# Performance work log

Measured on AMD Instinct MI355X. Metric: run time of the kernel, lower is better.

## Reference

```python
import jax, jax.numpy as jnp
import numpy as np

N = 100000        # nodes
E = 1600000       # edges (before self-loops)
IN_CH = 256       # input features
HEADS = 8         # conv1 heads; per-head dim also 8 (GATConv(in, heads, heads=heads))
HID = 8
NCLASS = 64
SLOPE = 0.2       # PyG leaky_relu negative slope


def _gat_conv(x, edge_index, W, att_src, att_dst, bias, heads, ch, concat):
    """PyG GATConv (eval mode): gather -> leaky_relu score -> segment softmax -> scatter."""
    n = x.shape[0]
    src, dst = edge_index[0], edge_index[1]
    h = (x @ W).reshape(n, heads, ch)                      # [N, H, C]
    a_src = jnp.einsum('nhc,hc->nh', h, att_src)           # [N, H]
    a_dst = jnp.einsum('nhc,hc->nh', h, att_dst)
    alpha = jax.nn.leaky_relu(a_src[src] + a_dst[dst], SLOPE)  # [E, H]
    # segment softmax over destination node
    amax = jax.ops.segment_max(alpha, dst, num_segments=n)     # [N, H]
    ex = jnp.exp(alpha - amax[dst])
    denom = jax.ops.segment_sum(ex, dst, num_segments=n)
    coef = ex / (denom[dst] + 1e-16)                           # [E, H]
    out = jax.ops.segment_sum(coef[:, :, None] * h[src], dst, num_segments=n)  # [N, H, C]
    if concat:
        out = out.reshape(n, heads * ch)
    else:
        out = out.mean(axis=1)
    return out + bias


def _add_self_loops(edge_index, n):
    loop = jnp.arange(n, dtype=edge_index.dtype)
    return jnp.concatenate([edge_index, jnp.stack([loop, loop])], axis=1)


def setup_inputs() -> dict:
    key = jax.random.key(0)
    ks = jax.random.split(key, 10)
    g = lambda k, shp, s: (jax.random.normal(k, shp, jnp.float32) * s)
    return {
        'x': jax.random.normal(ks[0], (N, IN_CH), jnp.float32),
        'edge_index': jax.random.randint(ks[1], (2, E), 0, N, dtype=jnp.int64),
        'W1': g(ks[2], (IN_CH, HEADS * HID), 1.0 / np.sqrt(IN_CH)),
        'att_src1': g(ks[3], (HEADS, HID), 0.3),
        'att_dst1': g(ks[4], (HEADS, HID), 0.3),
        'b1': jnp.zeros((HEADS * HID,), jnp.float32),
        'W2': g(ks[5], (HEADS * HID, NCLASS), 1.0 / np.sqrt(HEADS * HID)),
        'att_src2': g(ks[6], (1, NCLASS), 0.3),
        'att_dst2': g(ks[7], (1, NCLASS), 0.3),
        'b2': jnp.zeros((NCLASS,), jnp.float32),
    }


def reference(x, edge_index, W1, att_src1, att_dst1, b1, W2, att_src2, att_dst2, b2):
    ei = _add_self_loops(edge_index, x.shape[0])
    h = jax.nn.elu(_gat_conv(x, ei, W1, att_src1, att_dst1, b1, HEADS, HID, True))
    # dropout is a no-op in eval mode
    h = _gat_conv(h, ei, W2, att_src2, att_dst2, b2, 1, NCLASS, False)
    return jax.nn.log_softmax(h, axis=-1)
```

## Files before the change

### kernel.cpp

```cpp
#include <hip/hip_runtime.h>
#include <hip/hip_bf16.h>

#define LRELU_SLOPE 0.2f
#define NBUK 256
#define BCAP 9728
#define CH2 6144

typedef unsigned int uint;
typedef unsigned short ushort;
typedef short bt8 __attribute__((ext_vector_type(8)));
typedef float fx4 __attribute__((ext_vector_type(4)));

__device__ __forceinline__ ushort f2bf(float f) {
    uint u = __float_as_uint(f);
    return (ushort)((u + 0x7FFF + ((u >> 16) & 1)) >> 16);
}
__device__ __forceinline__ float bf2f(ushort h) {
    return __uint_as_float(((uint)h) << 16);
}

#define ACC8(e, hv) \
    acc[0] += (e) * bf2f((ushort)((hv).x & 0xffff)); \
    acc[1] += (e) * bf2f((ushort)((hv).x >> 16));    \
    acc[2] += (e) * bf2f((ushort)((hv).y & 0xffff)); \
    acc[3] += (e) * bf2f((ushort)((hv).y >> 16));    \
    acc[4] += (e) * bf2f((ushort)((hv).z & 0xffff)); \
    acc[5] += (e) * bf2f((ushort)((hv).z >> 16));    \
    acc[6] += (e) * bf2f((ushort)((hv).w & 0xffff)); \
    acc[7] += (e) * bf2f((ushort)((hv).w >> 16));

__global__ __launch_bounds__(256) void prep_init(
    const float* __restrict__ W1, const float* __restrict__ W2,
    ushort* __restrict__ WT1, ushort* __restrict__ WT2, int* __restrict__ pcur)
{
    int t = threadIdx.x;
    int idx = blockIdx.x * 256 + t;
    if (blockIdx.x == 0) pcur[t] = t * BCAP;
    if (idx < 64 * 256) {
        int c = idx >> 8, k = idx & 255;
        WT1[idx] = f2bf(W1[k * 64 + c]);
    }
    int i2 = idx - 64 * 256;
    if (i2 >= 0 && i2 < 64 * 64) {
        int c = i2 >> 6, k = i2 & 63;
        WT2[i2] = f2bf(W2[k * 64 + c]);
    }
}

__device__ __forceinline__ void partition_body(
    int bid, const int* __restrict__ ei, int E_, int ET,
    int* __restrict__ pcur, uint* __restrict__ pairs,
    int* lcnt, int* lsc, int* lplace, int* gpos)
{
    const int t = threadIdx.x;
    const int base = bid * CH2;
    const int total = min(CH2, ET - base);
    if (total <= 0) return;

    if (t < NBUK) lcnt[t] = 0;
    __syncthreads();

    uint pp[6]; int pk[6];
    #pragma unroll
    for (int i = 0; i < 6; ++i) {
        int idx = t + i * 1024;
        pk[i] = -1;
        if (idx < total) {
            int e = base + idx;
            int s, d;
            if (e < E_) { s = ei[e]; d = ei[E_ + e]; } else { s = d = e - E_; }
            pk[i] = d >> 9;
            pp[i] = (uint)s | ((uint)(d & 511) << 17);
            atomicAdd(&lcnt[pk[i]], 1);
        }
    }
    __syncthreads();

    if (t < NBUK) lsc[t] = lcnt[t];
    __syncthreads();
    for (int off = 1; off < NBUK; off <<= 1) {
        int add = 0;
        if (t < NBUK && t >= off) add = lsc[t - off];
        __syncthreads();
        if (t < NBUK) lsc[t] += add;
        __syncthreads();
    }
    if (t < NBUK) {
        int excl = lsc[t] - lcnt[t];
        lplace[t] = excl;
        int c = lcnt[t];
        gpos[t] = c ? (atomicAdd(&pcur[t], c) - excl) : 0;
    }
    __syncthreads();

    #pragma unroll
    for (int i = 0; i < 6; ++i) {
        if (pk[i] >= 0) {
            int slot = atomicAdd(&lplace[pk[i]], 1);
            pairs[gpos[pk[i]] + slot] = pp[i];
        }
    }
}

__device__ __forceinline__ void gemm1_body4(
    int gbid, const float* __restrict__ X, const ushort* __restrict__ WT,
    ushort* __restrict__ OUT, float* __restrict__ a_src, float* __restrict__ a_dst,
    const float* __restrict__ att_s, const float* __restrict__ att_d, int nrows,
    ushort* wt_l, ushort* a_l)
{
    constexpr int K = 256, LDW = K + 8, NIT = K / 32;
    const int t = threadIdx.x;
    const int tt = t & 255;
    const int base = (gbid * 4 + (t >> 8)) * 64;

    for (int idx = t * 8; idx < 64 * K; idx += 1024 * 8) {
        int r = idx / K, c = idx % K;
        *(uint4*)&wt_l[r * LDW + c] = *(const uint4*)&WT[idx];
    }

    const int w = tt >> 6, l = tt & 63;
    const int frow = l & 15;
    const int kof = (l >> 4) * 8;
    fx4 acc[4] = {};
    float4 rv0, rv1;

    auto load_tile = [&](int k0) {
        int kq = (tt & 7) * 4;
        int r0 = (tt >> 3);
        int g0 = base + r0, g1 = base + r0 + 32;
        rv0 = make_float4(0.f, 0.f, 0.f, 0.f);
        rv1 = make_float4(0.f, 0.f, 0.f, 0.f);
        if (g0 < nrows) rv0 = *(const float4*)(X + (size_t)g0 * K + k0 + kq);
        if (g1 < nrows) rv1 = *(const float4*)(X + (size_t)g1 * K + k0 + kq);
    };
    auto store_tile = [&]() {
        int kq = (tt & 7) * 4;
        int r0 = (tt >> 3);
        ushort4 o0, o1;
        o0.x = f2bf(rv0.x); o0.y = f2bf(rv0.y); o0.z = f2bf(rv0.z); o0.w = f2bf(rv0.w);
        o1.x = f2bf(rv1.x); o1.y = f2bf(rv1.y); o1.z = f2bf(rv1.z); o1.w = f2bf(rv1.w);
        *(ushort4*)&a_l[r0 * 40 + kq] = o0;
        *(ushort4*)&a_l[(r0 + 32) * 40 + kq] = o1;
    };

    load_tile(0);
    store_tile();
    for (int it = 0; it < NIT; ++it) {
        if (it + 1 < NIT) load_tile((it + 1) * 32);
        __syncthreads();
        bt8 af = *(const bt8*)&a_l[(16 * w + frow) * 40 + kof];
        #pragma unroll
        for (int g = 0; g < 4; ++g) {
            bt8 bf = *(const bt8*)&wt_l[(16 * g + frow) * LDW + it * 32 + kof];
            acc[g] = __builtin_amdgcn_mfma_f32_16x16x32_bf16(af, bf, acc[g], 0, 0, 0);
        }
        __syncthreads();
        if (it + 1 < NIT) store_tile();
    }

    const int orow0 = base + 16 * w + (l >> 4) * 4;
    const int ocol = l & 15;
    #pragma unroll
    for (int g = 0; g < 4; ++g) {
        #pragma unroll
        for (int r4 = 0; r4 < 4; ++r4) {
            int gr = orow0 + r4;
            if (gr < nrows) OUT[(size_t)gr * 64 + 16 * g + ocol] = f2bf(acc[g][r4]);
        }
    }

    float as_c[4], ad_c[4];
    #pragma unroll
    for (int g = 0; g < 4; ++g) {
        as_c[g] = att_s[16 * g + ocol];
        ad_c[g] = att_d[16 * g + ocol];
    }
    #pragma unroll
    for (int r4 = 0; r4 < 4; ++r4) {
        int gr = orow0 + r4;
        #pragma unroll
        for (int g = 0; g < 4; ++g) {
            float ps = acc[g][r4] * as_c[g];
            float pd = acc[g][r4] * ad_c[g];
            ps += __shfl_xor(ps, 1, 64); pd += __shfl_xor(pd, 1, 64);
            ps += __shfl_xor(ps, 2, 64); pd += __shfl_xor(pd, 2, 64);
            ps += __shfl_xor(ps, 4, 64); pd += __shfl_xor(pd, 4, 64);
            if ((l & 7) == 0 && gr < nrows) {
                int head = 2 * g + ((l >> 3) & 1);
                a_src[(size_t)gr * 8 + head] = ps;
                a_dst[(size_t)gr * 8 + head] = pd;
            }
        }
    }
}

__global__ __launch_bounds__(1024) void part_gemm1(
    const int* __restrict__ ei, int E_, int ET, int part_grid,
    int* __restrict__ pcur, uint* __restrict__ pairs,
    const float* __restrict__ x, const ushort* __restrict__ WT1,
    ushort* __restrict__ HB, float* __restrict__ a_s1, float* __restrict__ a_d1,
    const float* __restrict__ att_s, const float* __restrict__ att_d, int n)
{
    __shared__ int lcnt[NBUK], lsc[NBUK], lplace[NBUK], gpos[NBUK];
    __shared__ ushort wt_l[64 * 264];
    __shared__ ushort a_l4[4][64 * 40];
    if ((int)blockIdx.x < part_grid)
        partition_body(blockIdx.x, ei, E_, ET, pcur, pairs, lcnt, lsc, lplace, gpos);
    else
        gemm1_body4(blockIdx.x - part_grid, x, WT1, HB, a_s1, a_d1,
                    att_s, att_d, n, wt_l, a_l4[threadIdx.x >> 8]);
}

__global__ __launch_bounds__(1024) void phase2_build(
    const uint* __restrict__ pairs, const int* __restrict__ pcur,
    int* __restrict__ rp, int* __restrict__ ssrc, int n, int nbuk_used)
{
    __shared__ int hist[512], cur[512], psc[NBUK];
    const int k = blockIdx.x;
    const int t = threadIdx.x;
    const int beg = k * BCAP;
    const int cnt = pcur[k] - beg;
    const int dbase = k << 9;

    if (t < 512) hist[t] = 0;
    if (t < NBUK) psc[t] = (t < nbuk_used) ? (pcur[t] - t * BCAP) : 0;
    __syncthreads();
    for (int off = 1; off < NBUK; off <<= 1) {
        int add = (t < NBUK && t >= off) ? psc[t - off] : 0;
        __syncthreads();
        if (t < NBUK) psc[t] += add;
        __syncthreads();
    }
    const int bbase = k ? psc[k - 1] : 0;

    for (int i = t; i < cnt; i += 1024)
        atomicAdd(&hist[pairs[beg + i] >> 17], 1);
    __syncthreads();

    int c0 = (t < 512) ? hist[t] : 0;
    for (int off = 1; off < 512; off <<= 1) {
        int add = (t < 512 && t >= off) ? hist[t - off] : 0;
        __syncthreads();
        if (t < 512) hist[t] += add;
        __syncthreads();
    }
    if (t < 512) {
        int node = dbase + t;
        if (node < n) rp[node] = bbase + hist[t];
        cur[t] = hist[t] - c0;
    }
    __syncthreads();

    for (int i = t; i < cnt; i += 1024) {
        uint p = pairs[beg + i];
        int j = p >> 17;
        int pos = bbase + atomicAdd(&cur[j], 1);
        ssrc[pos] = (int)(p & 0x1FFFF);
    }
}

__global__ __launch_bounds__(256) void gemm2_att(
    const ushort* __restrict__ X, const ushort* __restrict__ WT,
    ushort* __restrict__ OUT, float* __restrict__ a_src, float* __restrict__ a_dst,
    const float* __restrict__ att_s, const float* __restrict__ att_d, int nrows)
{
    constexpr int K = 64, LDW = K + 8, NIT = K / 32;
    __shared__ ushort wt_l[64 * LDW];
    __shared__ ushort a_l[64 * 40];
    const int t = threadIdx.x;
    const int base = blockIdx.x * 64;

    for (int idx = t * 8; idx < 64 * K; idx += 256 * 8) {
        int r = idx / K, c = idx % K;
        *(uint4*)&wt_l[r * LDW + c] = *(const uint4*)&WT[idx];
    }

    const int w = t >> 6, l = t & 63;
    const int frow = l & 15;
    const int kof = (l >> 4) * 8;
    fx4 acc[4] = {};
    uint4 rb;

    auto load_tile = [&](int k0) {
        int r = t >> 2, kq = (t & 3) * 8;
        int gr = base + r;
        rb = make_uint4(0, 0, 0, 0);
        if (gr < nrows) rb = *(const uint4*)(X + (size_t)gr * K + k0 + kq);
    };
    auto store_tile = [&]() {
        int r = t >> 2, kq = (t & 3) * 8;
        *(uint4*)&a_l[r * 40 + kq] = rb;
    };

    load_tile(0);
    store_tile();
    for (int it = 0; it < NIT; ++it) {
        if (it + 1 < NIT) load_tile((it + 1) * 32);
        __syncthreads();
        bt8 af = *(const bt8*)&a_l[(16 * w + frow) * 40 + kof];
        #pragma unroll
        for (int g = 0; g < 4; ++g) {
            bt8 bf = *(const bt8*)&wt_l[(16 * g + frow) * LDW + it * 32 + kof];
            acc[g] = __builtin_amdgcn_mfma_f32_16x16x32_bf16(af, bf, acc[g], 0, 0, 0);
        }
        __syncthreads();
        if (it + 1 < NIT) store_tile();
    }

    const int orow0 = base + 16 * w + (l >> 4) * 4;
    const int ocol = l & 15;
    #pragma unroll
    for (int g = 0; g < 4; ++g) {
        #pragma unroll
        for (int r4 = 0; r4 < 4; ++r4) {
            int gr = orow0 + r4;
            if (gr < nrows) OUT[(size_t)gr * 64 + 16 * g + ocol] = f2bf(acc[g][r4]);
        }
    }

    float as_c[4], ad_c[4];
    #pragma unroll
    for (int g = 0; g < 4; ++g) {
        as_c[g] = att_s[16 * g + ocol];
        ad_c[g] = att_d[16 * g + ocol];
    }
    #pragma unroll
    for (int r4 = 0; r4 < 4; ++r4) {
        int gr = orow0 + r4;
        float ps = 0.f, pd = 0.f;
        #pragma unroll
        for (int g = 0; g < 4; ++g) {
            ps += acc[g][r4] * as_c[g];
            pd += acc[g][r4] * ad_c[g];
        }
        ps += __shfl_xor(ps, 1, 64); pd += __shfl_xor(pd, 1, 64);
        ps += __shfl_xor(ps, 2, 64); pd += __shfl_xor(pd, 2, 64);
        ps += __shfl_xor(ps, 4, 64); pd += __shfl_xor(pd, 4, 64);
        ps += __shfl_xor(ps, 8, 64); pd += __shfl_xor(pd, 8, 64);
        if ((l & 15) == 0 && gr < nrows) {
            a_src[gr] = ps;
            a_dst[gr] = pd;
        }
    }
}

__global__ __launch_bounds__(256) void gather_h8(
    const int* __restrict__ rp, const int* __restrict__ ssrc,
    const float* __restrict__ a_src, const float* __restrict__ a_dst,
    const ushort* __restrict__ HB, const float* __restrict__ bias,
    ushort* __restrict__ HACT, int n)
{
    int node = blockIdx.x * 32 + (threadIdx.x >> 3);
    if (node >= n) return;
    int ol = threadIdx.x & 7;
    int end = rp[node];
    int start = node ? rp[node - 1] : 0;
    float adh = a_dst[(size_t)node * 8 + ol];
    float acc[8] = {};
    float dsum = 0.f;

    int i0 = start;
    for (; i0 + 16 <= end; i0 += 16) {
        int svA = ssrc[i0 + ol];
        int svB = ssrc[i0 + 8 + ol];
        #pragma unroll
        for (int j = 0; j < 8; ++j) {
            int sjA = __shfl(svA, j, 8);
            float aA = a_src[(size_t)sjA * 8 + ol] + adh;
            aA = aA > 0.f ? aA : LRELU_SLOPE * aA;
            float eA = __expf(aA);
            uint4 hvA = *(const uint4*)(HB + (size_t)sjA * 64 + ol * 8);
            dsum += eA; ACC8(eA, hvA);
            int sjB = __shfl(svB, j, 8);
            float aB = a_src[(size_t)sjB * 8 + ol] + adh;
            aB = aB > 0.f ? aB : LRELU_SLOPE * aB;
            float eB = __expf(aB);
            uint4 hvB = *(const uint4*)(HB + (size_t)sjB * 64 + ol * 8);
            dsum += eB; ACC8(eB, hvB);
        }
    }
    for (; i0 < end; i0 += 8) {
        int cnt = min(8, end - i0);
        int sv = (ol < cnt) ? ssrc[i0 + ol] : 0;
        #pragma unroll
        for (int j = 0; j < 8; ++j) {
            int sj = __shfl(sv, j, 8);
            float a = a_src[(size_t)sj * 8 + ol] + adh;
            a = a > 0.f ? a : LRELU_SLOPE * a;
            float e = __expf(a);
            e = (j < cnt) ? e : 0.f;
            uint4 hv = *(const uint4*)(HB + (size_t)sj * 64 + ol * 8);
            dsum += e; ACC8(e, hv);
        }
    }
    float inv = 1.f / (dsum + 1e-16f);
    float4 b0 = *(const float4*)(bias + ol * 8);
    float4 b1 = *(const float4*)(bias + ol * 8 + 4);
    float v[8];
    v[0] = acc[0] * inv + b0.x; v[1] = acc[1] * inv + b0.y;
    v[2] = acc[2] * inv + b0.z; v[3] = acc[3] * inv + b0.w;
    v[4] = acc[4] * inv + b1.x; v[5] = acc[5] * inv + b1.y;
    v[6] = acc[6] * inv + b1.z; v[7] = acc[7] * inv + b1.w;
    #pragma unroll
    for (int c = 0; c < 8; ++c) v[c] = v[c] > 0.f ? v[c] : expm1f(v[c]);
    uint4 o;
    o.x = (uint)f2bf(v[0]) | ((uint)f2bf(v[1]) << 16);
    o.y = (uint)f2bf(v[2]) | ((uint)f2bf(v[3]) << 16);
    o.z = (uint)f2bf(v[4]) | ((uint)f2bf(v[5]) << 16);
    o.w = (uint)f2bf(v[6]) | ((uint)f2bf(v[7]) << 16);
    *(uint4*)(HACT + (size_t)node * 64 + ol * 8) = o;
}

__global__ __launch_bounds__(256) void gather_h1_lsm(
    const int* __restrict__ rp, const int* __restrict__ ssrc,
    const float* __restrict__ a_src, const float* __restrict__ a_dst,
    const ushort* __restrict__ HB, const float* __restrict__ bias,
    float* __restrict__ OUT, int n)
{
    int node = blockIdx.x * 32 + (threadIdx.x >> 3);
    if (node >= n) return;
    int ol = threadIdx.x & 7;
    int end = rp[node];
    int start = node ? rp[node - 1] : 0;
    float ad = a_dst[node];
    float acc[8] = {};
    float dsum = 0.f;

    int i0 = start;
    for (; i0 + 16 <= end; i0 += 16) {
        int svA = ssrc[i0 + ol];
        int svB = ssrc[i0 + 8 + ol];
        #pragma unroll
        for (int j = 0; j < 8; ++j) {
            int sjA = __shfl(svA, j, 8);
            float aA = a_src[sjA] + ad;
            aA = aA > 0.f ? aA : LRELU_SLOPE * aA;
            float eA = __expf(aA);
            uint4 hvA = *(const uint4*)(HB + (size_t)sjA * 64 + ol * 8);
            dsum += eA; ACC8(eA, hvA);
            int sjB = __shfl(svB, j, 8);
            float aB = a_src[sjB] + ad;
            aB = aB > 0.f ? aB : LRELU_SLOPE * aB;
            float eB = __expf(aB);
            uint4 hvB = *(const uint4*)(HB + (size_t)sjB * 64 + ol * 8);
            dsum += eB; ACC8(eB, hvB);
        }
    }
    for (; i0 < end; i0 += 8) {
        int cnt = min(8, end - i0);
        int sv = (ol < cnt) ? ssrc[i0 + ol] : 0;
        #pragma unroll
        for (int j = 0; j < 8; ++j) {
            int sj = __shfl(sv, j, 8);
            float a = a_src[sj] + ad;
            a = a > 0.f ? a : LRELU_SLOPE * a;
            float e = __expf(a);
            e = (j < cnt) ? e : 0.f;
            uint4 hv = *(const uint4*)(HB + (size_t)sj * 64 + ol * 8);
            dsum += e; ACC8(e, hv);
        }
    }
    float inv = 1.f / (dsum + 1e-16f);
    float4 b0 = *(const float4*)(bias + ol * 8);
    float4 b1 = *(const float4*)(bias + ol * 8 + 4);
    float v[8];
    v[0] = acc[0] * inv + b0.x; v[1] = acc[1] * inv + b0.y;
    v[2] = acc[2] * inv + b0.z; v[3] = acc[3] * inv + b0.w;
    v[4] = acc[4] * inv + b1.x; v[5] = acc[5] * inv + b1.y;
    v[6] = acc[6] * inv + b1.z; v[7] = acc[7] * inv + b1.w;

    float m = v[0];
    #pragma unroll
    for (int c = 1; c < 8; ++c) m = fmaxf(m, v[c]);
    m = fmaxf(m, __shfl_xor(m, 1, 8));
    m = fmaxf(m, __shfl_xor(m, 2, 8));
    m = fmaxf(m, __shfl_xor(m, 4, 8));
    float s = 0.f;
    #pragma unroll
    for (int c = 0; c < 8; ++c) s += __expf(v[c] - m);
    s += __shfl_xor(s, 1, 8);
    s += __shfl_xor(s, 2, 8);
    s += __shfl_xor(s, 4, 8);
    float lse = m + __logf(s);
    float4 o0 = make_float4(v[0] - lse, v[1] - lse, v[2] - lse, v[3] - lse);
    float4 o1 = make_float4(v[4] - lse, v[5] - lse, v[6] - lse, v[7] - lse);
    *(float4*)(OUT + (size_t)node * 64 + ol * 8) = o0;
    *(float4*)(OUT + (size_t)node * 64 + ol * 8 + 4) = o1;
}

extern "C" void kernel_launch(void* const* d_in, const int* in_sizes, int n_in,
                              void* d_out, int out_size, void* d_ws, size_t ws_size,
                              hipStream_t stream)
{
    const float* x    = (const float*)d_in[0];
    const int*   ei   = (const int*)d_in[1];
    const float* W1   = (const float*)d_in[2];
    const float* as1w = (const float*)d_in[3];
    const float* ad1w = (const float*)d_in[4];
    const float* b1   = (const float*)d_in[5];
    const float* W2   = (const float*)d_in[6];
    const float* as2w = (const float*)d_in[7];
    const float* ad2w = (const float*)d_in[8];
    const float* b2   = (const float*)d_in[9];
    float* out = (float*)d_out;

    const int n  = in_sizes[0] / 256;
    const int E_ = in_sizes[1] / 2;
    const int ET = E_ + n;
    const int NBUKU = (n + 511) >> 9;

    char* wsb = (char*)d_ws;
    uint*   pairs= (uint*)wsb;
    ushort* HB   = (ushort*)(pairs + (size_t)NBUK*BCAP);
    ushort* HACT = HB + (size_t)n * 64;
    float*  a_s1 = (float*)(HACT + (size_t)n * 64);
    float*  a_d1 = a_s1 + (size_t)n * 8;
    float*  a_s2 = a_d1 + (size_t)n * 8;
    float*  a_d2 = a_s2 + n;
    int*    rp   = (int*)(a_d2 + n);
    int*    pcur = rp + n;
    int*    ssrc = pcur + NBUK;
    ushort* WT1  = (ushort*)(ssrc + ET);
    ushort* WT2  = WT1 + 64 * 256;

    const int gemm_grid  = (n + 63) / 64;
    const int gemm_grid4 = (n + 255) / 256;
    const int gath_grid  = (n + 31) / 32;
    const int part_grid  = (ET + CH2 - 1) / CH2;

    prep_init<<<80, 256, 0, stream>>>(W1, W2, WT1, WT2, pcur);
    part_gemm1<<<part_grid + gemm_grid4, 1024, 0, stream>>>(
        ei, E_, ET, part_grid, pcur, pairs, x, WT1, HB, a_s1, a_d1, as1w, ad1w, n);
    phase2_build<<<NBUKU, 1024, 0, stream>>>(pairs, pcur, rp, ssrc, n, NBUKU);
    gather_h8<<<gath_grid, 256, 0, stream>>>(rp, ssrc, a_s1, a_d1, HB, b1, HACT, n);
    gemm2_att<<<gemm_grid, 256, 0, stream>>>(HACT, WT2, HB, a_s2, a_d2, as2w, ad2w, n);
    gather_h1_lsm<<<gath_grid, 256, 0, stream>>>(rp, ssrc, a_s2, a_d2, HB, b2, out, n);
}
```

Measured before the change: 179.3 us.

## Recompute layer-1 source attention scores from gathered features instead of storing them

The GEMM1 epilogue no longer computes or writes per-node a_src scores. Instead, gather_h8 recomputes each edge's source score as a dot product of the already-loaded bf16 feature row with att_src. This removes one random 32-byte-per-edge gather of a_src (and its write), trading it for extra ALU work per edge. It also uses bf16-rounded features for the score, which slightly changes numerics. The gather loop is simplified to 8-edge steps, and launch bounds request 8 blocks per CU.

```diff
diff --git a/kernel.cpp b/kernel.cpp
--- a/kernel.cpp
+++ b/kernel.cpp
@@ -28,6 +28,21 @@
     acc[5] += (e) * bf2f((ushort)((hv).z >> 16));    \
     acc[6] += (e) * bf2f((ushort)((hv).w & 0xffff)); \
     acc[7] += (e) * bf2f((ushort)((hv).w >> 16));
+
+#define EDGE_H8(sjv, LIVE) { \
+    uint4 hv = *(const uint4*)(HB + (size_t)(sjv) * 64 + ol * 8); \
+    float h0 = bf2f((ushort)(hv.x & 0xffff)), h1 = bf2f((ushort)(hv.x >> 16)); \
+    float h2 = bf2f((ushort)(hv.y & 0xffff)), h3 = bf2f((ushort)(hv.y >> 16)); \
+    float h4 = bf2f((ushort)(hv.z & 0xffff)), h5 = bf2f((ushort)(hv.z >> 16)); \
+    float h6 = bf2f((ushort)(hv.w & 0xffff)), h7 = bf2f((ushort)(hv.w >> 16)); \
+    float dt = h0*w0.x + h1*w0.y + h2*w0.z + h3*w0.w \
+             + h4*w1.x + h5*w1.y + h6*w1.z + h7*w1.w; \
+    float a_ = dt + adh; a_ = a_ > 0.f ? a_ : LRELU_SLOPE * a_; \
+    float e = __expf(a_); \
+    if (!(LIVE)) e = 0.f; \
+    dsum += e; \
+    acc[0] += e*h0; acc[1] += e*h1; acc[2] += e*h2; acc[3] += e*h3; \
+    acc[4] += e*h4; acc[5] += e*h5; acc[6] += e*h6; acc[7] += e*h7; }
 
 __global__ __launch_bounds__(256) void prep_init(
     const float* __restrict__ W1, const float* __restrict__ W2,
@@ -104,8 +119,8 @@
 
 __device__ __forceinline__ void gemm1_body4(
     int gbid, const float* __restrict__ X, const ushort* __restrict__ WT,
-    ushort* __restrict__ OUT, float* __restrict__ a_src, float* __restrict__ a_dst,
-    const float* __restrict__ att_s, const float* __restrict__ att_d, int nrows,
+    ushort* __restrict__ OUT, float* __restrict__ a_dst,
+    const float* __restrict__ att_d, int nrows,
     ushort* wt_l, ushort* a_l)
 {
     constexpr int K = 256, LDW = K + 8, NIT = K / 32;
@@ -169,25 +184,20 @@
         }
     }
 
-    float as_c[4], ad_c[4];
-    #pragma unroll
-    for (int g = 0; g < 4; ++g) {
-        as_c[g] = att_s[16 * g + ocol];
-        ad_c[g] = att_d[16 * g + ocol];
-    }
+    float ad_c[4];
+    #pragma unroll
+    for (int g = 0; g < 4; ++g) ad_c[g] = att_d[16 * g + ocol];
     #pragma unroll
     for (int r4 = 0; r4 < 4; ++r4) {
         int gr = orow0 + r4;
         #pragma unroll
         for (int g = 0; g < 4; ++g) {
-            float ps = acc[g][r4] * as_c[g];
             float pd = acc[g][r4] * ad_c[g];
-            ps += __shfl_xor(ps, 1, 64); pd += __shfl_xor(pd, 1, 64);
-            ps += __shfl_xor(ps, 2, 64); pd += __shfl_xor(pd, 2, 64);
-            ps += __shfl_xor(ps, 4, 64); pd += __shfl_xor(pd, 4, 64);
+            pd += __shfl_xor(pd, 1, 64);
+            pd += __shfl_xor(pd, 2, 64);
+            pd += __shfl_xor(pd, 4, 64);
             if ((l & 7) == 0 && gr < nrows) {
                 int head = 2 * g + ((l >> 3) & 1);
-                a_src[(size_t)gr * 8 + head] = ps;
                 a_dst[(size_t)gr * 8 + head] = pd;
             }
         }
@@ -198,8 +208,8 @@
     const int* __restrict__ ei, int E_, int ET, int part_grid,
     int* __restrict__ pcur, uint* __restrict__ pairs,
     const float* __restrict__ x, const ushort* __restrict__ WT1,
-    ushort* __restrict__ HB, float* __restrict__ a_s1, float* __restrict__ a_d1,
-    const float* __restrict__ att_s, const float* __restrict__ att_d, int n)
+    ushort* __restrict__ HB, float* __restrict__ a_d1,
+    const float* __restrict__ att_d, int n)
 {
     __shared__ int lcnt[NBUK], lsc[NBUK], lplace[NBUK], gpos[NBUK];
     __shared__ ushort wt_l[64 * 264];
@@ -207,8 +217,8 @@
     if ((int)blockIdx.x < part_grid)
         partition_body(blockIdx.x, ei, E_, ET, pcur, pairs, lcnt, lsc, lplace, gpos);
     else
-        gemm1_body4(blockIdx.x - part_grid, x, WT1, HB, a_s1, a_d1,
-                    att_s, att_d, n, wt_l, a_l4[threadIdx.x >> 8]);
+        gemm1_body4(blockIdx.x - part_grid, x, WT1, HB, a_d1,
+                    att_d, n, wt_l, a_l4[threadIdx.x >> 8]);
 }
 
 __global__ __launch_bounds__(1024) void phase2_build(
@@ -344,9 +354,9 @@
     }
 }
 
-__global__ __launch_bounds__(256) void gather_h8(
+__global__ __launch_bounds__(256, 8) void gather_h8(
     const int* __restrict__ rp, const int* __restrict__ ssrc,
-    const float* __restrict__ a_src, const float* __restrict__ a_dst,
+    const float* __restrict__ a_dst, const float* __restrict__ att_s,
     const ushort* __restrict__ HB, const float* __restrict__ bias,
     ushort* __restrict__ HACT, int n)
 {
@@ -356,41 +366,27 @@
     int end = rp[node];
     int start = node ? rp[node - 1] : 0;
     float adh = a_dst[(size_t)node * 8 + ol];
+    float4 w0 = *(const float4*)(att_s + ol * 8);
+    float4 w1 = *(const float4*)(att_s + ol * 8 + 4);
     float acc[8] = {};
     float dsum = 0.f;
 
     int i0 = start;
-    for (; i0 + 16 <= end; i0 += 16) {
-        int svA = ssrc[i0 + ol];
-        int svB = ssrc[i0 + 8 + ol];
-        #pragma unroll
-        for (int j = 0; j < 8; ++j) {
-            int sjA = __shfl(svA, j, 8);
-            float aA = a_src[(size_t)sjA * 8 + ol] + adh;
-            aA = aA > 0.f ? aA : LRELU_SLOPE * aA;
-            float eA = __expf(aA);
-            uint4 hvA = *(const uint4*)(HB + (size_t)sjA * 64 + ol * 8);
-            dsum += eA; ACC8(eA, hvA);
-            int sjB = __shfl(svB, j, 8);
-            float aB = a_src[(size_t)sjB * 8 + ol] + adh;
-            aB = aB > 0.f ? aB : LRELU_SLOPE * aB;
-            float eB = __expf(aB);
-            uint4 hvB = *(const uint4*)(HB + (size_t)sjB * 64 + ol * 8);
-            dsum += eB; ACC8(eB, hvB);
-        }
-    }
-    for (; i0 < end; i0 += 8) {
-        int cnt = min(8, end - i0);
-        int sv = (ol < cnt) ? ssrc[i0 + ol] : 0;
+    for (; i0 + 8 <= end; i0 += 8) {
+        int sv = ssrc[i0 + ol];
         #pragma unroll
         for (int j = 0; j < 8; ++j) {
             int sj = __shfl(sv, j, 8);
-            float a = a_src[(size_t)sj * 8 + ol] + adh;
-            a = a > 0.f ? a : LRELU_SLOPE * a;
-            float e = __expf(a);
-            e = (j < cnt) ? e : 0.f;
-            uint4 hv = *(const uint4*)(HB + (size_t)sj * 64 + ol * 8);
-            dsum += e; ACC8(e, hv);
+            EDGE_H8(sj, true);
+        }
+    }
+    if (i0 < end) {
+        int cnt = end - i0;
+        int sv = (ol < cnt) ? ssrc[i0 + ol] : 0;
+        #pragma unroll
+        for (int j = 0; j < 8; ++j) {
+            int sj = __shfl(sv, j, 8);
+            EDGE_H8(sj, j < cnt);
         }
     }
     float inv = 1.f / (dsum + 1e-16f);
@@ -513,8 +509,7 @@
     uint*   pairs= (uint*)wsb;
     ushort* HB   = (ushort*)(pairs + (size_t)NBUK*BCAP);
     ushort* HACT = HB + (size_t)n * 64;
-    float*  a_s1 = (float*)(HACT + (size_t)n * 64);
-    float*  a_d1 = a_s1 + (size_t)n * 8;
+    float*  a_d1 = (float*)(HACT + (size_t)n * 64);
     float*  a_s2 = a_d1 + (size_t)n * 8;
     float*  a_d2 = a_s2 + n;
     int*    rp   = (int*)(a_d2 + n);
@@ -530,9 +525,9 @@
 
     prep_init<<<80, 256, 0, stream>>>(W1, W2, WT1, WT2, pcur);
     part_gemm1<<<part_grid + gemm_grid4, 1024, 0, stream>>>(
-        ei, E_, ET, part_grid, pcur, pairs, x, WT1, HB, a_s1, a_d1, as1w, ad1w, n);
+        ei, E_, ET, part_grid, pcur, pairs, x, WT1, HB, a_d1, ad1w, n);
     phase2_build<<<NBUKU, 1024, 0, stream>>>(pairs, pcur, rp, ssrc, n, NBUKU);
-    gather_h8<<<gath_grid, 256, 0, stream>>>(rp, ssrc, a_s1, a_d1, HB, b1, HACT, n);
+    gather_h8<<<gath_grid, 256, 0, stream>>>(rp, ssrc, a_d1, as1w, HB, b1, HACT, n);
     gemm2_att<<<gemm_grid, 256, 0, stream>>>(HACT, WT2, HB, a_s2, a_d2, as2w, ad2w, n);
     gather_h1_lsm<<<gath_grid, 256, 0, stream>>>(rp, ssrc, a_s2, a_d2, HB, b2, out, n);
 }
```

After: 255.8 us. 1.43x slower.
